# Kernel tuning notes

Measured on AMD Instinct MI355X. Metric: run time of the kernel, lower is better.

Reference implementation:

```python
import jax, jax.numpy as jnp
import numpy as np

BATCH_SIZE = 512
N_PARTS = 4
TEMP_FAC = 0.1
D = 4096
EPS = 1e-6


def _static_indices():
    # bs and factor per the n_parts==4, batch_size!=12 branch
    bs = 4 * BATCH_SIZE
    factor = 10 * N_PARTS
    pos = np.arange(bs)
    active = pos[pos % (3 * N_PARTS) < N_PARTS]            # positions that contribute
    # i1..i6 = (pos + k*n_parts) % bs for k = 0..5
    I = (active[:, None] + np.arange(6)[None, :] * N_PARTS) % bs   # (P, 6)
    # denominator indices removed: (pos + k*n_parts) % bs for k = 0..factor*n_parts-1
    offs = (active[:, None] + np.arange(factor * N_PARTS)[None, :] * N_PARTS) % bs
    M = np.ones((active.shape[0], bs), dtype=np.float32)
    M[np.arange(active.shape[0])[:, None], offs] = 0.0     # (P, bs) denominator mask
    return I, M

_I, _M = _static_indices()
# symmetrical-loss pairs: (i1,i2),(i2,i3),(i1,i4),(i4,i5),(i5,i6),(i2,i5),(i3,i6)
_PAIRS = [(0, 1), (1, 2), (0, 3), (3, 4), (4, 5), (1, 4), (2, 5)]


def setup_inputs() -> dict:
    key = jax.random.key(0)
    reg_pred = jax.random.normal(key, (4 * BATCH_SIZE, D), dtype=jnp.float32)
    return {"reg_pred": reg_pred}


def reference(reg_pred):
    I = jnp.asarray(_I)
    M = jnp.asarray(_M)
    norms = jnp.linalg.norm(reg_pred, axis=1)              # (bs,)
    # torch CosineSimilarity: dot / max(||a||*||b||, eps)
    gram = reg_pred @ reg_pred.T                           # (bs, bs)
    S = gram / jnp.maximum(norms[:, None] * norms[None, :], EPS) / TEMP_FAC
    E = jnp.exp(S)                                         # (bs, bs)
    # denominator exp-sums for each anchor role k at each active position p
    Dsum = jnp.einsum('pkb,pb->pk', E[I], M)               # (P, 6)
    total = jnp.float32(0.0)
    for a, b in _PAIRS:
        num = S[I[:, a], I[:, b]]                          # (P,)
        en = jnp.exp(num)
        total = total + jnp.sum(-jnp.log(en / (en + Dsum[:, a]))
                                - jnp.log(en / (en + Dsum[:, b])))
    return total / (6 * BATCH_SIZE)
```

## Files before the change

kernel.cpp:

```cpp
#include <hip/hip_runtime.h>
#include <hip/hip_bf16.h>
#include <stdint.h>

#define NROWS 2048
#define DIM   4096
#define NACT  684
#define INV_TEMP 10.0f
#define NTILE 136
#define KSPLIT 4
#define KSEG  1024
#define KIT   16
#define FP8_SCALE 16.0f
#define PART_SCALE (1.0f / 256.0f)

#define WAITCNT_VM0   0x0F70
#define WAITCNT_VM4   0x0F74
#define WAITCNT_VM8   0x0F78
#define WAITCNT_VM12  0x0F7C

typedef __attribute__((ext_vector_type(4))) float floatx4;
typedef __attribute__((ext_vector_type(16))) float floatx16;
typedef __attribute__((ext_vector_type(4))) int intx4;
typedef __attribute__((ext_vector_type(8))) int intx8;
typedef __attribute__((ext_vector_type(8))) short shortx8;
typedef __attribute__((ext_vector_type(8))) unsigned short ushortx8;

static __device__ __forceinline__ unsigned short f32_to_bf16(float f) {
  union { float f; unsigned int u; } v; v.f = f;
  unsigned int u = v.u;
  unsigned int r = u + 0x7fffu + ((u >> 16) & 1u);
  return (unsigned short)(r >> 16);
}
static __device__ __forceinline__ float bf16_to_f32(unsigned short u) {
  union { unsigned int u; float f; } v; v.u = ((unsigned int)u) << 16;
  return v.f;
}
static __device__ __forceinline__ unsigned short f32_to_f16(float f) {
  _Float16 h = (_Float16)f;
  union { _Float16 h; unsigned short u; } v; v.h = h;
  return v.u;
}
static __device__ __forceinline__ float f16_to_f32(unsigned short u) {
  union { unsigned short u; _Float16 h; } v; v.u = u;
  return (float)v.h;
}

__global__ __launch_bounds__(256) void k_normconv_fp8(const float* __restrict__ X,
                                                      unsigned char* __restrict__ Yq,
                                                      float* __restrict__ T,
                                                      float* __restrict__ out) {
  const int row = blockIdx.x;
  if (threadIdx.x == 0) T[row] = 0.f;
  if (row == 0 && threadIdx.x == 64) *out = 0.f;
  const float4* xr = (const float4*)(X + (size_t)row * DIM);
  float4 v[4];
  float s = 0.f;
#pragma unroll
  for (int t = 0; t < 4; t++) {
    float4 w = xr[threadIdx.x * 4 + t];
    v[t] = w;
    s += w.x * w.x + w.y * w.y + w.z * w.z + w.w * w.w;
  }
#pragma unroll
  for (int off = 32; off > 0; off >>= 1) s += __shfl_down(s, off, 64);
  __shared__ float wsum[4];
  if ((threadIdx.x & 63) == 0) wsum[threadIdx.x >> 6] = s;
  __syncthreads();
  const float total = wsum[0] + wsum[1] + wsum[2] + wsum[3];
  const float sc = FP8_SCALE / fmaxf(sqrtf(total), 1e-30f);
  uint4 o;
  unsigned int r0;
  r0 = __builtin_amdgcn_cvt_pk_fp8_f32(v[0].x * sc, v[0].y * sc, 0, false);
  o.x = __builtin_amdgcn_cvt_pk_fp8_f32(v[0].z * sc, v[0].w * sc, r0, true);
  r0 = __builtin_amdgcn_cvt_pk_fp8_f32(v[1].x * sc, v[1].y * sc, 0, false);
  o.y = __builtin_amdgcn_cvt_pk_fp8_f32(v[1].z * sc, v[1].w * sc, r0, true);
  r0 = __builtin_amdgcn_cvt_pk_fp8_f32(v[2].x * sc, v[2].y * sc, 0, false);
  o.z = __builtin_amdgcn_cvt_pk_fp8_f32(v[2].z * sc, v[2].w * sc, r0, true);
  r0 = __builtin_amdgcn_cvt_pk_fp8_f32(v[3].x * sc, v[3].y * sc, 0, false);
  o.w = __builtin_amdgcn_cvt_pk_fp8_f32(v[3].z * sc, v[3].w * sc, r0, true);
  ((uint4*)(Yq + (size_t)row * DIM))[threadIdx.x] = o;
}

__global__ __launch_bounds__(256) void k_gemm_mx(const unsigned char* __restrict__ Yq,
                                                 unsigned short* __restrict__ P) {
  __shared__ __attribute__((aligned(16))) unsigned char lds[4 * 16384];
  const int bid = blockIdx.x;
  const int kz = bid & 3;
  const int t  = bid >> 2;
  int ti = 0, rem = t;
  while (rem >= 16 - ti) { rem -= 16 - ti; ti++; }
  const int tj = ti + rem;
  const int row0 = ti * 128;
  const int col0 = tj * 128;
  const int kbase = kz * KSEG;

  const int tid  = threadIdx.x;
  const int lane = tid & 63;
  const int wave = tid >> 6;
  const int wr = wave >> 1;
  const int wc = wave & 1;

  floatx16 zero = {0.f, 0.f, 0.f, 0.f, 0.f, 0.f, 0.f, 0.f,
                   0.f, 0.f, 0.f, 0.f, 0.f, 0.f, 0.f, 0.f};
  floatx16 acc[2][2];
#pragma unroll
  for (int i = 0; i < 2; i++)
#pragma unroll
    for (int j = 0; j < 2; j++) acc[i][j] = zero;

  const int r2  = tid >> 2;
  const int c16 = tid & 3;
  const unsigned int swst = (unsigned)(((r2 >> 1) & 3) << 4);
  const unsigned int colst = ((unsigned)(c16 << 4)) ^ swst;
  const unsigned char* gA = Yq + (size_t)(row0 + r2) * DIM + kbase + colst;
  const unsigned char* gB = Yq + (size_t)(col0 + r2) * DIM + kbase + colst;

#define ISSUE(st, koff)                                                                  \
  do {                                                                                   \
    __builtin_amdgcn_global_load_lds(                                                    \
        (const __attribute__((address_space(1))) void*)(gA + (koff)),                    \
        (__attribute__((address_space(3))) void*)(lds + (st) * 16384 + tid * 16),        \
        16, 0, 0);                                                                       \
    __builtin_amdgcn_global_load_lds(                                                    \
        (const __attribute__((address_space(1))) void*)(gA + (size_t)64 * DIM + (koff)), \
        (__attribute__((address_space(3))) void*)(lds + (st) * 16384 + 4096 + tid * 16), \
        16, 0, 0);                                                                       \
    __builtin_amdgcn_global_load_lds(                                                    \
        (const __attribute__((address_space(1))) void*)(gB + (koff)),                    \
        (__attribute__((address_space(3))) void*)(lds + (st) * 16384 + 8192 + tid * 16), \
        16, 0, 0);                                                                       \
    __builtin_amdgcn_global_load_lds(                                                    \
        (const __attribute__((address_space(1))) void*)(gB + (size_t)64 * DIM + (koff)), \
        (__attribute__((address_space(3))) void*)(lds + (st) * 16384 + 12288 + tid * 16),\
        16, 0, 0);                                                                       \
  } while (0)

#define COMPUTE(st)                                                                      \
  do {                                                                                   \
    const unsigned char* bA = lds + (st) * 16384;                                        \
    const unsigned char* bB = bA + 8192;                                                 \
    const unsigned int c0 = (unsigned)((lane >> 5) << 5);                                \
    intx8 af[2], bf[2];                                                                  \
    _Pragma("unroll")                                                                    \
    for (int mi = 0; mi < 2; mi++) {                                                     \
      const int r = wr * 64 + mi * 32 + (lane & 31);                                     \
      const unsigned int sw = (unsigned)(((r >> 1) & 3) << 4);                           \
      const unsigned char* base = bA + r * 64;                                           \
      intx4 lo = *(const intx4*)(base + (c0 ^ sw));                                      \
      intx4 hi = *(const intx4*)(base + ((c0 ^ sw) ^ 16u));                              \
      intx8 v;                                                                           \
      v[0] = lo[0]; v[1] = lo[1]; v[2] = lo[2]; v[3] = lo[3];                            \
      v[4] = hi[0]; v[5] = hi[1]; v[6] = hi[2]; v[7] = hi[3];                            \
      af[mi] = v;                                                                        \
    }                                                                                    \
    _Pragma("unroll")                                                                    \
    for (int ni = 0; ni < 2; ni++) {                                                     \
      const int r = wc * 64 + ni * 32 + (lane & 31);                                     \
      const unsigned int sw = (unsigned)(((r >> 1) & 3) << 4);                           \
      const unsigned char* base = bB + r * 64;                                           \
      intx4 lo = *(const intx4*)(base + (c0 ^ sw));                                      \
      intx4 hi = *(const intx4*)(base + ((c0 ^ sw) ^ 16u));                              \
      intx8 v;                                                                           \
      v[0] = lo[0]; v[1] = lo[1]; v[2] = lo[2]; v[3] = lo[3];                            \
      v[4] = hi[0]; v[5] = hi[1]; v[6] = hi[2]; v[7] = hi[3];                            \
      bf[ni] = v;                                                                        \
    }                                                                                    \
    _Pragma("unroll")                                                                    \
    for (int mi = 0; mi < 2; mi++)                                                       \
      _Pragma("unroll")                                                                  \
      for (int ni = 0; ni < 2; ni++)                                                     \
        acc[mi][ni] = __builtin_amdgcn_mfma_scale_f32_32x32x64_f8f6f4(                   \
            af[mi], bf[ni], acc[mi][ni], 0, 0, 0, 0x7F7F7F7F, 0, 0x7F7F7F7F);            \
  } while (0)

  ISSUE(0, 0);
  ISSUE(1, 64);
  ISSUE(2, 128);
#pragma unroll 4
  for (int k = 0; k < KIT; k++) {
    const int cur = k & 3;
    if (k < KIT - 3) {
      ISSUE((k + 3) & 3, (k + 3) * 64);
      __builtin_amdgcn_s_waitcnt(WAITCNT_VM12);
    } else if (k == KIT - 3) {
      __builtin_amdgcn_s_waitcnt(WAITCNT_VM8);
    } else if (k == KIT - 2) {
      __builtin_amdgcn_s_waitcnt(WAITCNT_VM4);
    } else {
      __builtin_amdgcn_s_waitcnt(WAITCNT_VM0);
    }
    __builtin_amdgcn_sched_barrier(0);
    __builtin_amdgcn_s_barrier();
    COMPUTE(cur);
    if (k < KIT - 1) {
      __builtin_amdgcn_s_barrier();
      __builtin_amdgcn_sched_barrier(0);
    }
  }

#undef ISSUE
#undef COMPUTE

  unsigned short* dst = P + (size_t)(t * KSPLIT + kz) * 16384;
  const int cc = lane & 31;
  const int cr = (lane >> 5) * 4;
#pragma unroll
  for (int mi = 0; mi < 2; mi++) {
#pragma unroll
    for (int ni = 0; ni < 2; ni++) {
      const int col = wc * 64 + ni * 32 + cc;
#pragma unroll
      for (int q = 0; q < 4; q++) {
        const int row = wr * 64 + mi * 32 + q * 8 + cr;
        unsigned int d0 = (unsigned int)f32_to_bf16(acc[mi][ni][q * 4 + 0] * PART_SCALE) |
                          ((unsigned int)f32_to_bf16(acc[mi][ni][q * 4 + 1] * PART_SCALE) << 16);
        unsigned int d1 = (unsigned int)f32_to_bf16(acc[mi][ni][q * 4 + 2] * PART_SCALE) |
                          ((unsigned int)f32_to_bf16(acc[mi][ni][q * 4 + 3] * PART_SCALE) << 16);
        uint2 v; v.x = d0; v.y = d1;
        *(uint2*)(dst + (size_t)col * 128 + row) = v;
      }
    }
  }
}

__global__ __launch_bounds__(256) void k_combine(const unsigned short* __restrict__ P,
                                                 unsigned short* __restrict__ S,
                                                 float* __restrict__ T) {
  __shared__ float tileS[32][132];
  __shared__ float tileE[32][132];
  const int t = blockIdx.x;
  const int h = blockIdx.y;
  int ti = 0, rem = t;
  while (rem >= 16 - ti) { rem -= 16 - ti; ti++; }
  const int tj = ti + rem;
  const int gr = ti * 128, gc = tj * 128;
  const int c0 = h * 32;
  const int tid = threadIdx.x;
  const int cl = tid >> 3;
  const int q  = tid & 7;

  float acc[16];
#pragma unroll
  for (int j = 0; j < 16; j++) acc[j] = 0.f;
#pragma unroll
  for (int kz = 0; kz < KSPLIT; kz++) {
    const ushortx8* p = (const ushortx8*)(P + (size_t)(t * KSPLIT + kz) * 16384 +
                                          (size_t)(c0 + cl) * 128 + q * 16);
#pragma unroll
    for (int c = 0; c < 2; c++) {
      ushortx8 u = p[c];
#pragma unroll
      for (int e = 0; e < 8; e++) acc[c * 8 + e] += bf16_to_f32((unsigned short)u[e]);
    }
  }
  float cs = 0.f;
  unsigned short hv[16];
#pragma unroll
  for (int j = 0; j < 16; j++) {
    float v = acc[j] * INV_TEMP;
    float ev = __expf(v);
    hv[j] = f32_to_f16(v);
    tileS[cl][q * 16 + j] = v;
    tileE[cl][q * 16 + j] = ev;
    cs += ev;
  }
  {
    uint4* srow = (uint4*)(S + (size_t)(gc + c0 + cl) * NROWS + gr + q * 16);
#pragma unroll
    for (int u = 0; u < 2; u++) {
      uint4 w;
      w.x = (unsigned int)hv[u * 8 + 0] | ((unsigned int)hv[u * 8 + 1] << 16);
      w.y = (unsigned int)hv[u * 8 + 2] | ((unsigned int)hv[u * 8 + 3] << 16);
      w.z = (unsigned int)hv[u * 8 + 4] | ((unsigned int)hv[u * 8 + 5] << 16);
      w.w = (unsigned int)hv[u * 8 + 6] | ((unsigned int)hv[u * 8 + 7] << 16);
      srow[u] = w;
    }
  }
  cs += __shfl_xor(cs, 1, 64);
  cs += __shfl_xor(cs, 2, 64);
  cs += __shfl_xor(cs, 4, 64);
  if (q == 0) atomicAdd(&T[gc + c0 + cl], cs);

  if (ti != tj) {
    __syncthreads();
    const int r = tid >> 1;
    const int hh = tid & 1;
    float rs = 0.f;
    unsigned short hv2[16];
#pragma unroll
    for (int e = 0; e < 16; e++) {
      hv2[e] = f32_to_f16(tileS[hh * 16 + e][r]);
      rs += tileE[hh * 16 + e][r];
    }
    uint4* drow = (uint4*)(S + (size_t)(gr + r) * NROWS + gc + c0 + hh * 16);
#pragma unroll
    for (int u = 0; u < 2; u++) {
      uint4 w;
      w.x = (unsigned int)hv2[u * 8 + 0] | ((unsigned int)hv2[u * 8 + 1] << 16);
      w.y = (unsigned int)hv2[u * 8 + 2] | ((unsigned int)hv2[u * 8 + 3] << 16);
      w.z = (unsigned int)hv2[u * 8 + 4] | ((unsigned int)hv2[u * 8 + 5] << 16);
      w.w = (unsigned int)hv2[u * 8 + 6] | ((unsigned int)hv2[u * 8 + 7] << 16);
      drow[u] = w;
    }
    rs += __shfl_xor(rs, 1, 64);
    if (hh == 0) atomicAdd(&T[gr + r], rs);
  }
}

__global__ __launch_bounds__(384) void k_tail(const unsigned short* __restrict__ S,
                                              const float* __restrict__ T,
                                              float* __restrict__ out) {
  __shared__ float ds_s[6];
  const int p = blockIdx.x;
  const int a = 12 * (p >> 2) + (p & 3);
  const int tid = threadIdx.x;
  const int k = tid >> 6;
  const int lane = tid & 63;
  const int row = (a + 4 * k) & (NROWS - 1);
  const int m = a >> 2;
  const int c = a & 3;
  const uint2* sr = (const uint2*)(S + (size_t)row * NROWS);
  float s = 0.f;
  {
    uint2 v0 = sr[(m + lane) & 511];
    uint2 v1 = sr[(m + 64 + lane) & 511];
    unsigned short e0 = (c < 2) ? (unsigned short)(v0.x >> (16 * c))
                                : (unsigned short)(v0.y >> (16 * (c - 2)));
    unsigned short e1 = (c < 2) ? (unsigned short)(v1.x >> (16 * c))
                                : (unsigned short)(v1.y >> (16 * (c - 2)));
    s += __expf(f16_to_f32(e0)) + __expf(f16_to_f32(e1));
    if (lane < 32) {
      uint2 v2 = sr[(m + 128 + lane) & 511];
      unsigned short e2 = (c < 2) ? (unsigned short)(v2.x >> (16 * c))
                                  : (unsigned short)(v2.y >> (16 * (c - 2)));
      s += __expf(f16_to_f32(e2));
    }
  }
#pragma unroll
  for (int off = 32; off > 0; off >>= 1) s += __shfl_down(s, off, 64);
  if (lane == 0) ds_s[k] = T[row] - s;
  __syncthreads();

  float r = 0.f;
  if (tid < 7) {
    const int pa[7] = {0, 1, 0, 3, 4, 1, 2};
    const int pb[7] = {1, 2, 3, 4, 5, 4, 5};
    const int ra = (a + 4 * pa[tid]) & (NROWS - 1);
    const int rb = (a + 4 * pb[tid]) & (NROWS - 1);
    const float num = f16_to_f32(S[(size_t)ra * NROWS + rb]);
    const float en = __expf(num);
    r = __logf(en + ds_s[pa[tid]]) + __logf(en + ds_s[pb[tid]]) - 2.f * num;
  }
  if (tid < 64) {
    r += __shfl_down(r, 4, 64);
    r += __shfl_down(r, 2, 64);
    r += __shfl_down(r, 1, 64);
    if (tid == 0) atomicAdd(out, r * (1.0f / (6.0f * 512.0f)));
  }
}

__global__ __launch_bounds__(256) void k_normconv(const float* __restrict__ X,
                                                  unsigned short* __restrict__ Y) {
  const int row = blockIdx.x;
  const float4* xr = (const float4*)(X + (size_t)row * DIM);
  float4 v[4];
  float s = 0.f;
#pragma unroll
  for (int t = 0; t < 4; t++) {
    float4 w = xr[threadIdx.x + t * 256];
    v[t] = w;
    s += w.x * w.x + w.y * w.y + w.z * w.z + w.w * w.w;
  }
#pragma unroll
  for (int off = 32; off > 0; off >>= 1) s += __shfl_down(s, off, 64);
  __shared__ float wsum[4];
  if ((threadIdx.x & 63) == 0) wsum[threadIdx.x >> 6] = s;
  __syncthreads();
  const float total = wsum[0] + wsum[1] + wsum[2] + wsum[3];
  const float inv = 1.0f / fmaxf(sqrtf(total), 1e-30f);
  ushort4* yr = (ushort4*)(Y + (size_t)row * DIM);
#pragma unroll
  for (int t = 0; t < 4; t++) {
    float4 w = v[t];
    ushort4 o;
    o.x = f32_to_bf16(w.x * inv);
    o.y = f32_to_bf16(w.y * inv);
    o.z = f32_to_bf16(w.z * inv);
    o.w = f32_to_bf16(w.w * inv);
    yr[threadIdx.x + t * 256] = o;
  }
}

__global__ __launch_bounds__(256) void k_gemm(const unsigned short* __restrict__ Y,
                                              float* __restrict__ S) {
  __shared__ __attribute__((aligned(16))) unsigned short sA[128 * 32];
  __shared__ __attribute__((aligned(16))) unsigned short sB[128 * 32];
  const int tid  = threadIdx.x;
  const int lane = tid & 63;
  const int wave = tid >> 6;
  const int wr = wave >> 1;
  const int wc = wave & 1;
  const int row0 = blockIdx.y * 128;
  const int col0 = blockIdx.x * 128;

  floatx4 zero = {0.f, 0.f, 0.f, 0.f};
  floatx4 acc[4][4];
#pragma unroll
  for (int i = 0; i < 4; i++)
#pragma unroll
    for (int j = 0; j < 4; j++) acc[i][j] = zero;

  const int sr = tid >> 2;
  const int sc = (tid & 3) * 8;
  const unsigned short* gA0 = Y + (size_t)(row0 + sr) * DIM + sc;
  const unsigned short* gA1 = gA0 + (size_t)64 * DIM;
  const unsigned short* gB0 = Y + (size_t)(col0 + sr) * DIM + sc;
  const unsigned short* gB1 = gB0 + (size_t)64 * DIM;

  const int fr = lane & 15;
  const int fc = (lane >> 4) * 8;

  for (int k0 = 0; k0 < DIM; k0 += 32) {
    __builtin_amdgcn_global_load_lds(
        (const __attribute__((address_space(1))) void*)(gA0 + k0),
        (__attribute__((address_space(3))) void*)(sA + tid * 8), 16, 0, 0);
    __builtin_amdgcn_global_load_lds(
        (const __attribute__((address_space(1))) void*)(gA1 + k0),
        (__attribute__((address_space(3))) void*)(sA + 2048 + tid * 8), 16, 0, 0);
    __builtin_amdgcn_global_load_lds(
        (const __attribute__((address_space(1))) void*)(gB0 + k0),
        (__attribute__((address_space(3))) void*)(sB + tid * 8), 16, 0, 0);
    __builtin_amdgcn_global_load_lds(
        (const __attribute__((address_space(1))) void*)(gB1 + k0),
        (__attribute__((address_space(3))) void*)(sB + 2048 + tid * 8), 16, 0, 0);
    __syncthreads();

    shortx8 af[4], bf[4];
#pragma unroll
    for (int mi = 0; mi < 4; mi++)
      af[mi] = *(const shortx8*)(sA + (wr * 64 + mi * 16 + fr) * 32 + fc);
#pragma unroll
    for (int ni = 0; ni < 4; ni++)
      bf[ni] = *(const shortx8*)(sB + (wc * 64 + ni * 16 + fr) * 32 + fc);
#pragma unroll
    for (int mi = 0; mi < 4; mi++)
#pragma unroll
      for (int ni = 0; ni < 4; ni++)
        acc[mi][ni] = __builtin_amdgcn_mfma_f32_16x16x32_bf16(af[mi], bf[ni], acc[mi][ni], 0, 0, 0);
    __syncthreads();
  }

  const int cc  = lane & 15;
  const int cr4 = (lane >> 4) * 4;
#pragma unroll
  for (int mi = 0; mi < 4; mi++) {
    const int row = row0 + wr * 64 + mi * 16 + cr4;
#pragma unroll
    for (int ni = 0; ni < 4; ni++) {
      const int col = col0 + wc * 64 + ni * 16 + cc;
      float* dst = S + (size_t)row * NROWS + col;
#pragma unroll
      for (int r = 0; r < 4; r++) dst[(size_t)r * NROWS] = acc[mi][ni][r] * INV_TEMP;
    }
  }
}

__global__ __launch_bounds__(256) void k_rowsum(const float* __restrict__ S,
                                                float* __restrict__ T) {
  const int row = blockIdx.x;
  const float* sr = S + (size_t)row * NROWS;
  float s = 0.f;
  for (int b = threadIdx.x; b < NROWS; b += 256) s += __expf(sr[b]);
#pragma unroll
  for (int off = 32; off > 0; off >>= 1) s += __shfl_down(s, off, 64);
  __shared__ float wsum[4];
  if ((threadIdx.x & 63) == 0) wsum[threadIdx.x >> 6] = s;
  __syncthreads();
  if (threadIdx.x == 0) T[row] = wsum[0] + wsum[1] + wsum[2] + wsum[3];
}

__global__ __launch_bounds__(64) void k_dsum(const float* __restrict__ S,
                                             const float* __restrict__ T,
                                             float* __restrict__ Ds) {
  const int p = blockIdx.x;
  const int k = blockIdx.y;
  const int a = 12 * (p >> 2) + (p & 3);
  const int lane = threadIdx.x;
  const int row = (a + 4 * k) & (NROWS - 1);
  const int m = a >> 2;
  const int c = a & 3;
  const float4* sr4 = (const float4*)(S + (size_t)row * NROWS);
  float s = 0.f;
  {
    float4 v0 = sr4[(m + lane) & 511];
    float4 v1 = sr4[(m + 64 + lane) & 511];
    float e0 = c == 0 ? v0.x : c == 1 ? v0.y : c == 2 ? v0.z : v0.w;
    float e1 = c == 0 ? v1.x : c == 1 ? v1.y : c == 2 ? v1.z : v1.w;
    s += __expf(e0) + __expf(e1);
    if (lane < 32) {
      float4 v2 = sr4[(m + 128 + lane) & 511];
      float e2 = c == 0 ? v2.x : c == 1 ? v2.y : c == 2 ? v2.z : v2.w;
      s += __expf(e2);
    }
  }
#pragma unroll
  for (int off = 32; off > 0; off >>= 1) s += __shfl_down(s, off, 64);
  if (lane == 0) Ds[p * 6 + k] = T[row] - s;
}

__global__ __launch_bounds__(256) void k_final(const float* __restrict__ S,
                                               const float* __restrict__ Ds,
                                               float* __restrict__ out) {
  const int pa[7] = {0, 1, 0, 3, 4, 1, 2};
  const int pb[7] = {1, 2, 3, 4, 5, 4, 5};
  const int idx = blockIdx.x * 256 + threadIdx.x;
  float s = 0.f;
  if (idx < NACT * 7) {
    const int p = idx / 7;
    const int q = idx - p * 7;
    const int a0 = 12 * (p >> 2) + (p & 3);
    const int ra = (a0 + 4 * pa[q]) & (NROWS - 1);
    const int rb = (a0 + 4 * pb[q]) & (NROWS - 1);
    const float num = S[(size_t)ra * NROWS + rb];
    const float en = __expf(num);
    s = __logf(en + Ds[p * 6 + pa[q]]) + __logf(en + Ds[p * 6 + pb[q]]) - 2.f * num;
  }
#pragma unroll
  for (int off = 32; off > 0; off >>= 1) s += __shfl_down(s, off, 64);
  if ((threadIdx.x & 63) == 0) atomicAdd(out, s * (1.0f / (6.0f * 512.0f)));
}

extern "C" void kernel_launch(void* const* d_in, const int* in_sizes, int n_in,
                              void* d_out, int out_size, void* d_ws, size_t ws_size,
                              hipStream_t stream) {
  const float* X = (const float*)d_in[0];
  char* ws = (char*)d_ws;
  float* out = (float*)d_out;

  const size_t pOff = (size_t)32 * 1024 * 1024;
  const size_t pBytes = (size_t)NTILE * KSPLIT * 16384 * 2;
  const size_t needA = pOff + pBytes + 8192 + NACT * 6 * 4 + 256;

  if (ws_size >= needA) {
    unsigned char* Yq = (unsigned char*)ws;
    unsigned short* S16 = (unsigned short*)(ws + (size_t)16 * 1024 * 1024);
    unsigned short* P = (unsigned short*)(ws + pOff);
    float* T  = (float*)(ws + pOff + pBytes);
    hipLaunchKernelGGL(k_normconv_fp8, dim3(NROWS), dim3(256), 0, stream, X, Yq, T, out);
    hipLaunchKernelGGL(k_gemm_mx, dim3(NTILE * KSPLIT), dim3(256), 0, stream, Yq, P);
    hipLaunchKernelGGL(k_combine, dim3(NTILE, 4), dim3(256), 0, stream, P, S16, T);
    hipLaunchKernelGGL(k_tail, dim3(NACT), dim3(384), 0, stream, S16, T, out);
  } else {
    unsigned short* Y = (unsigned short*)ws;
    float* S = (float*)(ws + (size_t)16 * 1024 * 1024);
    float* T  = (float*)(ws + pOff);
    float* Ds = (float*)(ws + pOff + 8192);
    hipMemsetAsync(out, 0, sizeof(float), stream);
    hipLaunchKernelGGL(k_normconv, dim3(NROWS), dim3(256), 0, stream, X, Y);
    hipLaunchKernelGGL(k_gemm, dim3(16, 16), dim3(256), 0, stream, Y, S);
    hipLaunchKernelGGL(k_rowsum, dim3(NROWS), dim3(256), 0, stream, S, T);
    hipLaunchKernelGGL(k_dsum, dim3(NACT, 6), dim3(64), 0, stream, S, T, Ds);
    hipLaunchKernelGGL(k_final, dim3((NACT * 7 + 255) / 256), dim3(256), 0, stream, S, Ds, out);
  }
}
```

Before: 110.8 us.

## Fuse split-K combine into GEMM via last-arriver counter, remap blocks

The separate combine kernel is folded into the GEMM kernel. Each k-split block increments a per-tile atomic counter, and the last block to arrive reduces the four partials, computes exp and the row/column sums, and writes S. This removes one kernel launch and its gap, at the cost of serialising the combine onto one block per tile and adding fences and atomics. Block IDs are also remapped so that the k-splits of a tile are spread across XCDs. The fp8 normalisation kernel now uses strided coalesced loads with per-dword stores.

```diff
diff --git a/kernel.cpp b/kernel.cpp
--- a/kernel.cpp
+++ b/kernel.cpp
@@ -48,16 +48,18 @@
 __global__ __launch_bounds__(256) void k_normconv_fp8(const float* __restrict__ X,
                                                       unsigned char* __restrict__ Yq,
                                                       float* __restrict__ T,
-                                                      float* __restrict__ out) {
+                                                      float* __restrict__ out,
+                                                      int* __restrict__ cnt) {
   const int row = blockIdx.x;
   if (threadIdx.x == 0) T[row] = 0.f;
   if (row == 0 && threadIdx.x == 64) *out = 0.f;
+  if (row < NTILE && threadIdx.x == 128) cnt[row] = 0;
   const float4* xr = (const float4*)(X + (size_t)row * DIM);
   float4 v[4];
   float s = 0.f;
 #pragma unroll
   for (int t = 0; t < 4; t++) {
-    float4 w = xr[threadIdx.x * 4 + t];
+    float4 w = xr[threadIdx.x + t * 256];
     v[t] = w;
     s += w.x * w.x + w.y * w.y + w.z * w.z + w.w * w.w;
   }
@@ -68,23 +70,25 @@
   __syncthreads();
   const float total = wsum[0] + wsum[1] + wsum[2] + wsum[3];
   const float sc = FP8_SCALE / fmaxf(sqrtf(total), 1e-30f);
-  uint4 o;
-  unsigned int r0;
-  r0 = __builtin_amdgcn_cvt_pk_fp8_f32(v[0].x * sc, v[0].y * sc, 0, false);
-  o.x = __builtin_amdgcn_cvt_pk_fp8_f32(v[0].z * sc, v[0].w * sc, r0, true);
-  r0 = __builtin_amdgcn_cvt_pk_fp8_f32(v[1].x * sc, v[1].y * sc, 0, false);
-  o.y = __builtin_amdgcn_cvt_pk_fp8_f32(v[1].z * sc, v[1].w * sc, r0, true);
-  r0 = __builtin_amdgcn_cvt_pk_fp8_f32(v[2].x * sc, v[2].y * sc, 0, false);
-  o.z = __builtin_amdgcn_cvt_pk_fp8_f32(v[2].z * sc, v[2].w * sc, r0, true);
-  r0 = __builtin_amdgcn_cvt_pk_fp8_f32(v[3].x * sc, v[3].y * sc, 0, false);
-  o.w = __builtin_amdgcn_cvt_pk_fp8_f32(v[3].z * sc, v[3].w * sc, r0, true);
-  ((uint4*)(Yq + (size_t)row * DIM))[threadIdx.x] = o;
-}
-
-__global__ __launch_bounds__(256) void k_gemm_mx(const unsigned char* __restrict__ Yq,
-                                                 unsigned short* __restrict__ P) {
+  unsigned int* yr = (unsigned int*)(Yq + (size_t)row * DIM);
+#pragma unroll
+  for (int t = 0; t < 4; t++) {
+    float4 w = v[t];
+    unsigned int r0 = __builtin_amdgcn_cvt_pk_fp8_f32(w.x * sc, w.y * sc, 0, false);
+    r0 = __builtin_amdgcn_cvt_pk_fp8_f32(w.z * sc, w.w * sc, r0, true);
+    yr[threadIdx.x + t * 256] = r0;
+  }
+}
+
+__global__ __launch_bounds__(256) void k_gemm_fused(const unsigned char* __restrict__ Yq,
+                                                    unsigned short* __restrict__ P,
+                                                    unsigned short* __restrict__ S,
+                                                    float* __restrict__ T,
+                                                    int* __restrict__ cnt) {
   __shared__ __attribute__((aligned(16))) unsigned char lds[4 * 16384];
-  const int bid = blockIdx.x;
+  __shared__ int last_flag;
+  const int bid0 = blockIdx.x;
+  const int bid = (bid0 & 7) * 68 + (bid0 >> 3);
   const int kz = bid & 3;
   const int t  = bid >> 2;
   int ti = 0, rem = t;
@@ -201,109 +205,113 @@
 #undef ISSUE
 #undef COMPUTE
 
-  unsigned short* dst = P + (size_t)(t * KSPLIT + kz) * 16384;
-  const int cc = lane & 31;
-  const int cr = (lane >> 5) * 4;
-#pragma unroll
-  for (int mi = 0; mi < 2; mi++) {
-#pragma unroll
-    for (int ni = 0; ni < 2; ni++) {
-      const int col = wc * 64 + ni * 32 + cc;
-#pragma unroll
-      for (int q = 0; q < 4; q++) {
-        const int row = wr * 64 + mi * 32 + q * 8 + cr;
-        unsigned int d0 = (unsigned int)f32_to_bf16(acc[mi][ni][q * 4 + 0] * PART_SCALE) |
-                          ((unsigned int)f32_to_bf16(acc[mi][ni][q * 4 + 1] * PART_SCALE) << 16);
-        unsigned int d1 = (unsigned int)f32_to_bf16(acc[mi][ni][q * 4 + 2] * PART_SCALE) |
-                          ((unsigned int)f32_to_bf16(acc[mi][ni][q * 4 + 3] * PART_SCALE) << 16);
-        uint2 v; v.x = d0; v.y = d1;
-        *(uint2*)(dst + (size_t)col * 128 + row) = v;
+  {
+    unsigned short* dst = P + (size_t)(t * KSPLIT + kz) * 16384;
+    const int cc = lane & 31;
+    const int cr = (lane >> 5) * 4;
+#pragma unroll
+    for (int mi = 0; mi < 2; mi++) {
+#pragma unroll
+      for (int ni = 0; ni < 2; ni++) {
+        const int col = wc * 64 + ni * 32 + cc;
+#pragma unroll
+        for (int q = 0; q < 4; q++) {
+          const int row = wr * 64 + mi * 32 + q * 8 + cr;
+          unsigned int d0 = (unsigned int)f32_to_bf16(acc[mi][ni][q * 4 + 0] * PART_SCALE) |
+                            ((unsigned int)f32_to_bf16(acc[mi][ni][q * 4 + 1] * PART_SCALE) << 16);
+          unsigned int d1 = (unsigned int)f32_to_bf16(acc[mi][ni][q * 4 + 2] * PART_SCALE) |
+                            ((unsigned int)f32_to_bf16(acc[mi][ni][q * 4 + 3] * PART_SCALE) << 16);
+          uint2 v; v.x = d0; v.y = d1;
+          *(uint2*)(dst + (size_t)col * 128 + row) = v;
+        }
       }
     }
   }
-}
-
-__global__ __launch_bounds__(256) void k_combine(const unsigned short* __restrict__ P,
-                                                 unsigned short* __restrict__ S,
-                                                 float* __restrict__ T) {
-  __shared__ float tileS[32][132];
-  __shared__ float tileE[32][132];
-  const int t = blockIdx.x;
-  const int h = blockIdx.y;
-  int ti = 0, rem = t;
-  while (rem >= 16 - ti) { rem -= 16 - ti; ti++; }
-  const int tj = ti + rem;
+
+  __threadfence();
+  __syncthreads();
+  if (tid == 0) {
+    int old = __hip_atomic_fetch_add(&cnt[t], 1, __ATOMIC_ACQ_REL, __HIP_MEMORY_SCOPE_AGENT);
+    last_flag = (old == KSPLIT - 1) ? 1 : 0;
+  }
+  __syncthreads();
+  if (!last_flag) return;
+
+  float* tileS = (float*)lds;
+  float* tileE = (float*)(lds + 16896);
   const int gr = ti * 128, gc = tj * 128;
-  const int c0 = h * 32;
-  const int tid = threadIdx.x;
   const int cl = tid >> 3;
   const int q  = tid & 7;
 
-  float acc[16];
-#pragma unroll
-  for (int j = 0; j < 16; j++) acc[j] = 0.f;
-#pragma unroll
-  for (int kz = 0; kz < KSPLIT; kz++) {
-    const ushortx8* p = (const ushortx8*)(P + (size_t)(t * KSPLIT + kz) * 16384 +
-                                          (size_t)(c0 + cl) * 128 + q * 16);
-#pragma unroll
-    for (int c = 0; c < 2; c++) {
-      ushortx8 u = p[c];
-#pragma unroll
-      for (int e = 0; e < 8; e++) acc[c * 8 + e] += bf16_to_f32((unsigned short)u[e]);
-    }
-  }
-  float cs = 0.f;
-  unsigned short hv[16];
-#pragma unroll
-  for (int j = 0; j < 16; j++) {
-    float v = acc[j] * INV_TEMP;
-    float ev = __expf(v);
-    hv[j] = f32_to_f16(v);
-    tileS[cl][q * 16 + j] = v;
-    tileE[cl][q * 16 + j] = ev;
-    cs += ev;
-  }
-  {
-    uint4* srow = (uint4*)(S + (size_t)(gc + c0 + cl) * NROWS + gr + q * 16);
-#pragma unroll
-    for (int u = 0; u < 2; u++) {
-      uint4 w;
-      w.x = (unsigned int)hv[u * 8 + 0] | ((unsigned int)hv[u * 8 + 1] << 16);
-      w.y = (unsigned int)hv[u * 8 + 2] | ((unsigned int)hv[u * 8 + 3] << 16);
-      w.z = (unsigned int)hv[u * 8 + 4] | ((unsigned int)hv[u * 8 + 5] << 16);
-      w.w = (unsigned int)hv[u * 8 + 6] | ((unsigned int)hv[u * 8 + 7] << 16);
-      srow[u] = w;
-    }
-  }
-  cs += __shfl_xor(cs, 1, 64);
-  cs += __shfl_xor(cs, 2, 64);
-  cs += __shfl_xor(cs, 4, 64);
-  if (q == 0) atomicAdd(&T[gc + c0 + cl], cs);
-
-  if (ti != tj) {
-    __syncthreads();
-    const int r = tid >> 1;
-    const int hh = tid & 1;
-    float rs = 0.f;
-    unsigned short hv2[16];
-#pragma unroll
-    for (int e = 0; e < 16; e++) {
-      hv2[e] = f32_to_f16(tileS[hh * 16 + e][r]);
-      rs += tileE[hh * 16 + e][r];
-    }
-    uint4* drow = (uint4*)(S + (size_t)(gr + r) * NROWS + gc + c0 + hh * 16);
-#pragma unroll
-    for (int u = 0; u < 2; u++) {
-      uint4 w;
-      w.x = (unsigned int)hv2[u * 8 + 0] | ((unsigned int)hv2[u * 8 + 1] << 16);
-      w.y = (unsigned int)hv2[u * 8 + 2] | ((unsigned int)hv2[u * 8 + 3] << 16);
-      w.z = (unsigned int)hv2[u * 8 + 4] | ((unsigned int)hv2[u * 8 + 5] << 16);
-      w.w = (unsigned int)hv2[u * 8 + 6] | ((unsigned int)hv2[u * 8 + 7] << 16);
-      drow[u] = w;
-    }
-    rs += __shfl_xor(rs, 1, 64);
-    if (hh == 0) atomicAdd(&T[gr + r], rs);
+  for (int h = 0; h < 4; h++) {
+    if (h) __syncthreads();
+    const int c0 = h * 32;
+    float acc2[16];
+#pragma unroll
+    for (int j = 0; j < 16; j++) acc2[j] = 0.f;
+#pragma unroll
+    for (int kz2 = 0; kz2 < KSPLIT; kz2++) {
+      const ushortx8* p = (const ushortx8*)(P + (size_t)(t * KSPLIT + kz2) * 16384 +
+                                            (size_t)(c0 + cl) * 128 + q * 16);
+#pragma unroll
+      for (int c = 0; c < 2; c++) {
+        ushortx8 u = p[c];
+#pragma unroll
+        for (int e = 0; e < 8; e++) acc2[c * 8 + e] += bf16_to_f32((unsigned short)u[e]);
+      }
+    }
+    float cs = 0.f;
+    unsigned short hv[16];
+#pragma unroll
+    for (int j = 0; j < 16; j++) {
+      float v = acc2[j] * INV_TEMP;
+      float ev = __expf(v);
+      hv[j] = f32_to_f16(v);
+      tileS[cl * 132 + q * 16 + j] = v;
+      tileE[cl * 132 + q * 16 + j] = ev;
+      cs += ev;
+    }
+    {
+      uint4* srow = (uint4*)(S + (size_t)(gc + c0 + cl) * NROWS + gr + q * 16);
+#pragma unroll
+      for (int u = 0; u < 2; u++) {
+        uint4 w;
+        w.x = (unsigned int)hv[u * 8 + 0] | ((unsigned int)hv[u * 8 + 1] << 16);
+        w.y = (unsigned int)hv[u * 8 + 2] | ((unsigned int)hv[u * 8 + 3] << 16);
+        w.z = (unsigned int)hv[u * 8 + 4] | ((unsigned int)hv[u * 8 + 5] << 16);
+        w.w = (unsigned int)hv[u * 8 + 6] | ((unsigned int)hv[u * 8 + 7] << 16);
+        srow[u] = w;
+      }
+    }
+    cs += __shfl_xor(cs, 1, 64);
+    cs += __shfl_xor(cs, 2, 64);
+    cs += __shfl_xor(cs, 4, 64);
+    if (q == 0) atomicAdd(&T[gc + c0 + cl], cs);
+
+    if (ti != tj) {
+      __syncthreads();
+      const int r = tid >> 1;
+      const int hh = tid & 1;
+      float rs = 0.f;
+      unsigned short hv2[16];
+#pragma unroll
+      for (int e = 0; e < 16; e++) {
+        hv2[e] = f32_to_f16(tileS[(hh * 16 + e) * 132 + r]);
+        rs += tileE[(hh * 16 + e) * 132 + r];
+      }
+      uint4* drow = (uint4*)(S + (size_t)(gr + r) * NROWS + gc + c0 + hh * 16);
+#pragma unroll
+      for (int u = 0; u < 2; u++) {
+        uint4 w;
+        w.x = (unsigned int)hv2[u * 8 + 0] | ((unsigned int)hv2[u * 8 + 1] << 16);
+        w.y = (unsigned int)hv2[u * 8 + 2] | ((unsigned int)hv2[u * 8 + 3] << 16);
+        w.z = (unsigned int)hv2[u * 8 + 4] | ((unsigned int)hv2[u * 8 + 5] << 16);
+        w.w = (unsigned int)hv2[u * 8 + 6] | ((unsigned int)hv2[u * 8 + 7] << 16);
+        drow[u] = w;
+      }
+      rs += __shfl_xor(rs, 1, 64);
+      if (hh == 0) atomicAdd(&T[gr + r], rs);
+    }
   }
 }
 
@@ -546,9 +554,9 @@
     unsigned short* S16 = (unsigned short*)(ws + (size_t)16 * 1024 * 1024);
     unsigned short* P = (unsigned short*)(ws + pOff);
     float* T  = (float*)(ws + pOff + pBytes);
-    hipLaunchKernelGGL(k_normconv_fp8, dim3(NROWS), dim3(256), 0, stream, X, Yq, T, out);
-    hipLaunchKernelGGL(k_gemm_mx, dim3(NTILE * KSPLIT), dim3(256), 0, stream, Yq, P);
-    hipLaunchKernelGGL(k_combine, dim3(NTILE, 4), dim3(256), 0, stream, P, S16, T);
+    int* cnt  = (int*)(ws + pOff + pBytes + 8192);
+    hipLaunchKernelGGL(k_normconv_fp8, dim3(NROWS), dim3(256), 0, stream, X, Yq, T, out, cnt);
+    hipLaunchKernelGGL(k_gemm_fused, dim3(NTILE * KSPLIT), dim3(256), 0, stream, Yq, P, S16, T, cnt);
     hipLaunchKernelGGL(k_tail, dim3(NACT), dim3(384), 0, stream, S16, T, out);
   } else {
     unsigned short* Y = (unsigned short*)ws;
```

Result: slower. 215.8 us (+94.7%).

## Shrink GEMM LDS ring to three stages, remap blocks across XCDs, coalesce norm loads

Applied to the files above, without the earlier changes.

The fp8 GEMM prefetch ring drops from four LDS stages to three, cutting LDS use per block so more blocks can be resident, at the cost of a shallower prefetch distance. Block IDs are permuted with (bid&7)*68+(bid>>3), presumably so consecutive tiles spread across the XCDs for better L2 locality. The normalize/convert kernel switches to a strided access pattern so consecutive threads read adjacent float4s and write adjacent 32-bit fp8 words. The loop is fully unrolled so the modulo-3 stage indices become constants.

```diff
diff --git a/kernel.cpp b/kernel.cpp
--- a/kernel.cpp
+++ b/kernel.cpp
@@ -16,7 +16,6 @@
 #define WAITCNT_VM0   0x0F70
 #define WAITCNT_VM4   0x0F74
 #define WAITCNT_VM8   0x0F78
-#define WAITCNT_VM12  0x0F7C
 
 typedef __attribute__((ext_vector_type(4))) float floatx4;
 typedef __attribute__((ext_vector_type(16))) float floatx16;
@@ -57,7 +56,7 @@
   float s = 0.f;
 #pragma unroll
   for (int t = 0; t < 4; t++) {
-    float4 w = xr[threadIdx.x * 4 + t];
+    float4 w = xr[threadIdx.x + t * 256];
     v[t] = w;
     s += w.x * w.x + w.y * w.y + w.z * w.z + w.w * w.w;
   }
@@ -68,23 +67,21 @@
   __syncthreads();
   const float total = wsum[0] + wsum[1] + wsum[2] + wsum[3];
   const float sc = FP8_SCALE / fmaxf(sqrtf(total), 1e-30f);
-  uint4 o;
-  unsigned int r0;
-  r0 = __builtin_amdgcn_cvt_pk_fp8_f32(v[0].x * sc, v[0].y * sc, 0, false);
-  o.x = __builtin_amdgcn_cvt_pk_fp8_f32(v[0].z * sc, v[0].w * sc, r0, true);
-  r0 = __builtin_amdgcn_cvt_pk_fp8_f32(v[1].x * sc, v[1].y * sc, 0, false);
-  o.y = __builtin_amdgcn_cvt_pk_fp8_f32(v[1].z * sc, v[1].w * sc, r0, true);
-  r0 = __builtin_amdgcn_cvt_pk_fp8_f32(v[2].x * sc, v[2].y * sc, 0, false);
-  o.z = __builtin_amdgcn_cvt_pk_fp8_f32(v[2].z * sc, v[2].w * sc, r0, true);
-  r0 = __builtin_amdgcn_cvt_pk_fp8_f32(v[3].x * sc, v[3].y * sc, 0, false);
-  o.w = __builtin_amdgcn_cvt_pk_fp8_f32(v[3].z * sc, v[3].w * sc, r0, true);
-  ((uint4*)(Yq + (size_t)row * DIM))[threadIdx.x] = o;
+  unsigned int* yr = (unsigned int*)(Yq + (size_t)row * DIM);
+#pragma unroll
+  for (int t = 0; t < 4; t++) {
+    float4 w = v[t];
+    unsigned int r0 = __builtin_amdgcn_cvt_pk_fp8_f32(w.x * sc, w.y * sc, 0, false);
+    r0 = __builtin_amdgcn_cvt_pk_fp8_f32(w.z * sc, w.w * sc, r0, true);
+    yr[threadIdx.x + t * 256] = r0;
+  }
 }
 
 __global__ __launch_bounds__(256) void k_gemm_mx(const unsigned char* __restrict__ Yq,
                                                  unsigned short* __restrict__ P) {
-  __shared__ __attribute__((aligned(16))) unsigned char lds[4 * 16384];
-  const int bid = blockIdx.x;
+  __shared__ __attribute__((aligned(16))) unsigned char lds[3 * 16384];
+  const int bid0 = blockIdx.x;
+  const int bid = (bid0 & 7) * 68 + (bid0 >> 3);
   const int kz = bid & 3;
   const int t  = bid >> 2;
   int ti = 0, rem = t;
@@ -175,14 +172,11 @@
 
   ISSUE(0, 0);
   ISSUE(1, 64);
-  ISSUE(2, 128);
-#pragma unroll 4
+#pragma unroll
   for (int k = 0; k < KIT; k++) {
-    const int cur = k & 3;
-    if (k < KIT - 3) {
-      ISSUE((k + 3) & 3, (k + 3) * 64);
-      __builtin_amdgcn_s_waitcnt(WAITCNT_VM12);
-    } else if (k == KIT - 3) {
+    const int cur = k % 3;
+    if (k < KIT - 2) {
+      ISSUE((k + 2) % 3, (k + 2) * 64);
       __builtin_amdgcn_s_waitcnt(WAITCNT_VM8);
     } else if (k == KIT - 2) {
       __builtin_amdgcn_s_waitcnt(WAITCNT_VM4);
```

After: 112.4 us. No clear change (+1.5%).
